# Kernel optimization log

Hardware: AMD Instinct MI355X
Metric: run time of the kernel (lower is better)

The kernel has to match this reference:

```python
import jax, jax.numpy as jnp
import numpy as np

D = 1024
H = 16
HD = D // H
FF = 4096
B = 2
S = 2048


def _layer_norm(x, g, b, eps=1e-5):
    mu = jnp.mean(x, axis=-1, keepdims=True)
    var = jnp.mean(jnp.square(x - mu), axis=-1, keepdims=True)
    return (x - mu) * jax.lax.rsqrt(var + eps) * g + b


def setup_inputs() -> dict:
    key = jax.random.key(0)
    ks = jax.random.split(key, 16)
    s = 0.02
    return {
        "x": jax.random.normal(ks[0], (B, S, D), jnp.float32),
        "Wq": jax.random.normal(ks[1], (H, D, HD), jnp.float32) * s,
        "bq": jnp.zeros((H, HD), jnp.float32),
        "Wk": jax.random.normal(ks[2], (H, D, HD), jnp.float32) * s,
        "bk": jnp.zeros((H, HD), jnp.float32),
        "Wv": jax.random.normal(ks[3], (H, D, HD), jnp.float32) * s,
        "bv": jnp.zeros((H, HD), jnp.float32),
        "Wo": jax.random.normal(ks[4], (D, D), jnp.float32) * s,
        "bo": jnp.zeros((D,), jnp.float32),
        "W1": jax.random.normal(ks[5], (D, FF), jnp.float32) * s,
        "b1": jnp.zeros((FF,), jnp.float32),
        "W2": jax.random.normal(ks[6], (FF, D), jnp.float32) * s,
        "b2": jnp.zeros((D,), jnp.float32),
        "g1": jnp.ones((D,), jnp.float32),
        "be1": jnp.zeros((D,), jnp.float32),
        "g2": jnp.ones((D,), jnp.float32),
        "be2": jnp.zeros((D,), jnp.float32),
    }


def reference(x, Wq, bq, Wk, bk, Wv, bv, Wo, bo, W1, b1, W2, b2, g1, be1, g2, be2):
    b, s, d = x.shape
    # per-head projections (vectorized over heads)
    q = jnp.einsum("bsd,hde->bhse", x, Wq) + bq[None, :, None, :]
    k = jnp.einsum("bsd,hde->bhse", x, Wk) + bk[None, :, None, :]
    v = jnp.einsum("bsd,hde->bhse", x, Wv) + bv[None, :, None, :]
    # NOTE: source scales by 1/dim_k (not 1/sqrt(dim_k)) -- kept faithful
    scores = jnp.einsum("bhse,bhte->bhst", q, k) / jnp.asarray(HD, x.dtype)
    causal = jnp.tril(jnp.ones((s, s), bool))  # [S,S]
    scores = jnp.where(causal[None, None], scores, jnp.asarray(-jnp.inf, x.dtype))
    attn = jax.nn.softmax(scores, axis=-1)
    ctx = jnp.einsum("bhst,bhte->bhse", attn, v)  # [B,H,S,hd]
    ctx = jnp.transpose(ctx, (0, 2, 1, 3)).reshape(b, s, d)  # concat heads
    attn_out = ctx @ Wo + bo
    x = _layer_norm(x + attn_out, g1, be1)
    # feed-forward: linear -> exact GELU -> linear (dropout = eval identity)
    h = jax.nn.gelu(x @ W1 + b1, approximate=False)
    ff = h @ W2 + b2
    return _layer_norm(x + ff, g2, be2)
```

## Files before the change

kernel.cpp:

```cpp
#include <hip/hip_runtime.h>
#include <math.h>

constexpr int Dm  = 1024;
constexpr int Hh  = 16;
constexpr int HDm = 64;
constexpr int FFm = 4096;
constexpr int Bb  = 2;
constexpr int Sq  = 2048;
constexpr int Mm  = Bb * Sq;

typedef __attribute__((ext_vector_type(8))) short short8;
typedef __attribute__((ext_vector_type(4))) short short4v;
typedef __attribute__((ext_vector_type(4))) float f32x4;

#define AS1 __attribute__((address_space(1)))
#define AS3 __attribute__((address_space(3)))

constexpr float QSCALE = 0.022542110013890054f;

__device__ __forceinline__ unsigned short f2b(float f) {
    union { float f; unsigned u; } v; v.f = f;
    unsigned r = v.u + 0x7FFFu + ((v.u >> 16) & 1u);
    return (unsigned short)(r >> 16);
}

__global__ __launch_bounds__(256) void convert_x(const float* __restrict__ x,
                                                 short* __restrict__ xb) {
    int i = blockIdx.x * 256 + threadIdx.x;
    float4 v = ((const float4*)x)[i];
    short4v o;
    o[0] = (short)f2b(v.x); o[1] = (short)f2b(v.y);
    o[2] = (short)f2b(v.z); o[3] = (short)f2b(v.w);
    ((short4v*)xb)[i] = o;
}

__global__ __launch_bounds__(256) void transpose_to_bf16(
    const float* __restrict__ src, short* __restrict__ dst, int R, int C) {
    __shared__ float t[64][65];
    const int c0 = blockIdx.x * 64, r0 = blockIdx.y * 64;
    const int lc = threadIdx.x & 63, lr4 = threadIdx.x >> 6;
    #pragma unroll
    for (int p = 0; p < 16; ++p) {
        int rr = p * 4 + lr4;
        t[rr][lc] = src[(size_t)(r0 + rr) * C + c0 + lc];
    }
    __syncthreads();
    #pragma unroll
    for (int p = 0; p < 16; ++p) {
        int rr = p * 4 + lr4;
        dst[(size_t)(c0 + rr) * R + r0 + lc] = (short)f2b(t[lc][rr]);
    }
}

__global__ __launch_bounds__(256) void build_wqkv(
    const float* __restrict__ Wq, const float* __restrict__ Wk,
    const float* __restrict__ Wv, short* __restrict__ dst) {
    const int kt = blockIdx.x, h = blockIdx.y, which = blockIdx.z;
    const float* W = ((which == 0) ? Wq : (which == 1) ? Wk : Wv) +
                     (size_t)h * Dm * HDm;
    __shared__ float t[64][65];
    const int lc = threadIdx.x & 63, lr4 = threadIdx.x >> 6;
    #pragma unroll
    for (int p = 0; p < 16; ++p) {
        int kr = p * 4 + lr4;
        t[kr][lc] = W[(size_t)(kt * 64 + kr) * HDm + lc];
    }
    __syncthreads();
    const int nbase = which * 1024 + h * 64;
    #pragma unroll
    for (int p = 0; p < 16; ++p) {
        int e = p * 4 + lr4;
        dst[(size_t)(nbase + e) * Dm + kt * 64 + lc] = (short)f2b(t[lc][e]);
    }
}

__global__ __launch_bounds__(256) void build_bqkv(
    const float* __restrict__ bq, const float* __restrict__ bk,
    const float* __restrict__ bv, float* __restrict__ bcat) {
    int n = blockIdx.x * 256 + threadIdx.x;
    const float* s = (n < 1024) ? bq : (n < 2048) ? bk : bv;
    bcat[n] = s[n & 1023];
}

template<int EPI>
__global__ __launch_bounds__(512, 2) void gemm256(
    const short* __restrict__ A, const short* __restrict__ Bt,
    const float* __restrict__ bias,
    short* __restrict__ outb,
    short* __restrict__ qo, short* __restrict__ ko, short* __restrict__ vo,
    int K, int N, int NMT)
{
    __shared__ __align__(16) char lds[131072];
    char* const ldsA = lds;
    char* const ldsB = lds + 65536;
    const int tid = threadIdx.x;
    const int l = tid & 63, wv = tid >> 6;
    const int wm = wv >> 2, wn = wv & 3;
    const int lr = l & 15, lg = l >> 4;
    const int bid = blockIdx.x;
    const int m0 = (bid % NMT) * 256;
    const int n0 = (bid / NMT) * 256;
    const size_t KB = (size_t)K * 2;
    const int NT = K >> 6;

    const char* pA[2][2];
    const char* pB[2][2];
    #pragma unroll
    for (int i = 0; i < 2; ++i) {
        int c = tid + 512 * i;
        int rh = c >> 3, j = c & 7;
        int sw = (j ^ (rh & 7)) << 4;
        #pragma unroll
        for (int h = 0; h < 2; ++h) {
            pA[h][i] = (const char*)A + (size_t)(m0 + h * 128 + rh) * KB + sw;
            pB[h][i] = (const char*)Bt + (size_t)(n0 + h * 128 + rh) * KB + sw;
        }
    }
    const int dbase = tid * 16;

    f32x4 acc[8][4];
    f32x4 z4 = {0.f, 0.f, 0.f, 0.f};
    #pragma unroll
    for (int i = 0; i < 8; ++i)
        #pragma unroll
        for (int j = 0; j < 4; ++j) acc[i][j] = z4;

#define STAGE_B(h, nb) do {                                                     \
    char* _b = ldsB + ((nb) * 2 + (h)) * 16384;                                 \
    __builtin_amdgcn_global_load_lds((const AS1 void*)pB[h][0],                 \
        (AS3 void*)(_b + dbase), 16, 0, 0);                                     \
    __builtin_amdgcn_global_load_lds((const AS1 void*)pB[h][1],                 \
        (AS3 void*)(_b + dbase + 8192), 16, 0, 0);                              \
    pB[h][0] += 128; pB[h][1] += 128; } while (0)
#define STAGE_A(h, nb) do {                                                     \
    char* _a = ldsA + ((nb) * 2 + (h)) * 16384;                                 \
    __builtin_amdgcn_global_load_lds((const AS1 void*)pA[h][0],                 \
        (AS3 void*)(_a + dbase), 16, 0, 0);                                     \
    __builtin_amdgcn_global_load_lds((const AS1 void*)pA[h][1],                 \
        (AS3 void*)(_a + dbase + 8192), 16, 0, 0);                              \
    pA[h][0] += 128; pA[h][1] += 128; } while (0)

    STAGE_B(0, 0); STAGE_B(1, 0); STAGE_A(0, 0); STAGE_A(1, 0);
    asm volatile("s_waitcnt vmcnt(2)" ::: "memory");
    __builtin_amdgcn_s_barrier();
    __builtin_amdgcn_sched_barrier(0);

    const int swk0 = ((0 + lg) ^ (lr & 7)) << 4;
    const int swk1 = ((4 + lg) ^ (lr & 7)) << 4;

    for (int kt = 0; kt < NT; ++kt) {
        const int buf = kt & 1, nbuf = buf ^ 1;
        const bool more = (kt + 1 < NT);
        char* const Ah0 = ldsA + (buf * 2) * 16384;
        char* const Ah1 = ldsA + (buf * 2 + 1) * 16384;
        char* const Bh  = ldsB + (buf * 2 + (wn >> 1)) * 16384 + (wn & 1) * 8192;

        short8 bf[4][2];
        #pragma unroll
        for (int nf = 0; nf < 4; ++nf) {
            const char* bb = Bh + (nf * 16 + lr) * 128;
            bf[nf][0] = *(const short8*)(bb + swk0);
            bf[nf][1] = *(const short8*)(bb + swk1);
        }
        short8 af[2][2];

#define LOAD_A(p) do {                                                          \
    _Pragma("unroll")                                                           \
    for (int j2 = 0; j2 < 2; ++j2) {                                            \
        const int mf = 2 * (p) + j2;                                            \
        const char* ab = ((mf >> 2) ? Ah1 : Ah0) +                              \
                         ((mf & 3) * 32 + wm * 16 + lr) * 128;                  \
        af[j2][0] = *(const short8*)(ab + swk0);                                \
        af[j2][1] = *(const short8*)(ab + swk1);                                \
    } } while (0)

#define MFMA8(p) do {                                                           \
    _Pragma("unroll")                                                           \
    for (int j2 = 0; j2 < 2; ++j2)                                              \
        _Pragma("unroll")                                                       \
        for (int nf = 0; nf < 4; ++nf) {                                        \
            acc[2 * (p) + j2][nf] = __builtin_amdgcn_mfma_f32_16x16x32_bf16(    \
                af[j2][0], bf[nf][0], acc[2 * (p) + j2][nf], 0, 0, 0);          \
            acc[2 * (p) + j2][nf] = __builtin_amdgcn_mfma_f32_16x16x32_bf16(    \
                af[j2][1], bf[nf][1], acc[2 * (p) + j2][nf], 0, 0, 0);          \
        } } while (0)

        LOAD_A(0);
        if (more) STAGE_B(0, nbuf);
        __builtin_amdgcn_s_barrier();
        asm volatile("s_waitcnt lgkmcnt(0)" ::: "memory");
        __builtin_amdgcn_sched_barrier(0);
        __builtin_amdgcn_s_setprio(1);
        MFMA8(0);
        __builtin_amdgcn_s_setprio(0);
        __builtin_amdgcn_s_barrier();
        LOAD_A(1);
        if (more) STAGE_B(1, nbuf);
        __builtin_amdgcn_s_barrier();
        asm volatile("s_waitcnt lgkmcnt(0)" ::: "memory");
        __builtin_amdgcn_sched_barrier(0);
        __builtin_amdgcn_s_setprio(1);
        MFMA8(1);
        __builtin_amdgcn_s_setprio(0);
        if (more) asm volatile("s_waitcnt vmcnt(4)" ::: "memory");
        else      asm volatile("s_waitcnt vmcnt(0)" ::: "memory");
        __builtin_amdgcn_s_barrier();
        __builtin_amdgcn_sched_barrier(0);
        LOAD_A(2);
        if (more) STAGE_A(0, nbuf);
        __builtin_amdgcn_s_barrier();
        asm volatile("s_waitcnt lgkmcnt(0)" ::: "memory");
        __builtin_amdgcn_sched_barrier(0);
        __builtin_amdgcn_s_setprio(1);
        MFMA8(2);
        __builtin_amdgcn_s_setprio(0);
        __builtin_amdgcn_s_barrier();
        LOAD_A(3);
        if (more) STAGE_A(1, nbuf);
        __builtin_amdgcn_s_barrier();
        asm volatile("s_waitcnt lgkmcnt(0)" ::: "memory");
        __builtin_amdgcn_sched_barrier(0);
        __builtin_amdgcn_s_setprio(1);
        MFMA8(3);
        __builtin_amdgcn_s_setprio(0);
        asm volatile("s_waitcnt vmcnt(2)" ::: "memory");
        __builtin_amdgcn_s_barrier();
        __builtin_amdgcn_sched_barrier(0);
#undef LOAD_A
#undef MFMA8
    }

    #pragma unroll
    for (int mf = 0; mf < 8; ++mf) {
        #pragma unroll
        for (int nf = 0; nf < 4; ++nf) {
            const int n = n0 + wn * 64 + nf * 16 + lr;
            const int mB = m0 + mf * 32 + wm * 16 + lg * 4;
            if (EPI == 1) {
                #pragma unroll
                for (int r = 0; r < 4; ++r) {
                    float val = acc[mf][nf][r] + bias[n];
                    val = 0.5f * val * (1.0f + erff(val * 0.70710678118654752f));
                    outb[(size_t)(mB + r) * N + n] = (short)f2b(val);
                }
            } else {
                const int which = n >> 10, hh = (n >> 6) & 15, e = n & 63;
                const int bb2 = mB >> 11, ss = mB & 2047;
                if (which == 2) {
                    short4v pk;
                    #pragma unroll
                    for (int r = 0; r < 4; ++r)
                        pk[r] = (short)f2b(acc[mf][nf][r] + bias[n]);
                    *(short4v*)&vo[(((size_t)bb2 * Hh + hh) * HDm + e) * Sq + ss] = pk;
                } else {
                    short* o = (which == 0) ? qo : ko;
                    const float sc = (which == 0) ? QSCALE : 1.0f;
                    #pragma unroll
                    for (int r = 0; r < 4; ++r) {
                        float val = (acc[mf][nf][r] + bias[n]) * sc;
                        o[(((size_t)bb2 * Hh + hh) * Sq + ss + r) * HDm + e] = (short)f2b(val);
                    }
                }
            }
        }
    }
#undef STAGE_A
#undef STAGE_B
}

template<int EPI>
__global__ __launch_bounds__(256, 2) void gemm128dp(
    const short* __restrict__ A, const short* __restrict__ Bt,
    const float* __restrict__ bias, const float* __restrict__ res,
    float* __restrict__ outf, short* __restrict__ outb,
    int K, int N)
{
    __shared__ __align__(16) char lds[65536];
    char* const ldsA = lds;
    char* const ldsB = lds + 32768;
    const int tid = threadIdx.x;
    const int l = tid & 63, wv = tid >> 6;
    const int wr = wv >> 1, wc = wv & 1;
    const int lr = l & 15, lg = l >> 4;
    const int m0 = blockIdx.x * 128, n0 = blockIdx.y * 128;
    const size_t KB = (size_t)K * 2;
    const int NT = K >> 6;

    const int r0 = tid >> 3, jj = tid & 7;
    const int sw = (jj ^ (r0 & 7)) << 4;
    const char* aSrc[4]; const char* bSrc1[2]; const char* bSrc2[2];
    #pragma unroll
    for (int i = 0; i < 4; ++i)
        aSrc[i] = (const char*)A + (size_t)(m0 + r0 + 32 * i) * KB + sw;
    #pragma unroll
    for (int i = 0; i < 2; ++i) {
        bSrc1[i] = (const char*)Bt + (size_t)(n0 + r0 + 64 * i) * KB + sw;
        bSrc2[i] = (const char*)Bt + (size_t)(n0 + 32 + r0 + 64 * i) * KB + sw;
    }
    const int aDst0 = tid * 16;

#define STAGE_SA(nb) do {                                                       \
    char* _a = ldsA + (nb) * 16384;                                             \
    _Pragma("unroll")                                                           \
    for (int i = 0; i < 4; ++i) {                                               \
        __builtin_amdgcn_global_load_lds((const AS1 void*)aSrc[i],              \
            (AS3 void*)(_a + aDst0 + i * 4096), 16, 0, 0);                      \
        aSrc[i] += 128;                                                         \
    } } while (0)
#define STAGE_SB1(nb) do {                                                      \
    char* _b = ldsB + (nb) * 16384;                                             \
    _Pragma("unroll")                                                           \
    for (int i = 0; i < 2; ++i) {                                               \
        __builtin_amdgcn_global_load_lds((const AS1 void*)bSrc1[i],             \
            (AS3 void*)(_b + aDst0 + i * 8192), 16, 0, 0);                      \
        bSrc1[i] += 128;                                                        \
    } } while (0)
#define STAGE_SB2(nb) do {                                                      \
    char* _b = ldsB + (nb) * 16384 + 4096;                                      \
    _Pragma("unroll")                                                           \
    for (int i = 0; i < 2; ++i) {                                               \
        __builtin_amdgcn_global_load_lds((const AS1 void*)bSrc2[i],             \
            (AS3 void*)(_b + aDst0 + i * 8192), 16, 0, 0);                      \
        bSrc2[i] += 128;                                                        \
    } } while (0)

    f32x4 acc[4][4];
    f32x4 z4 = {0.f, 0.f, 0.f, 0.f};
    #pragma unroll
    for (int i = 0; i < 4; ++i)
        #pragma unroll
        for (int j = 0; j < 4; ++j) acc[i][j] = z4;

    STAGE_SA(0); STAGE_SB1(0); STAGE_SB2(0);
    asm volatile("s_waitcnt vmcnt(2)" ::: "memory");
    __builtin_amdgcn_s_barrier();
    __builtin_amdgcn_sched_barrier(0);

    const int swk0 = ((0 + lg) ^ (lr & 7)) << 4;
    const int swk1 = ((4 + lg) ^ (lr & 7)) << 4;

    for (int kt = 0; kt < NT; ++kt) {
        const int buf = kt & 1, nbuf = buf ^ 1;
        const bool more = (kt + 1 < NT);
        char* const Ab = ldsA + buf * 16384;
        char* const Bb = ldsB + buf * 16384;

        short8 af[4][2], bf[2][2];
        #pragma unroll
        for (int mf = 0; mf < 4; ++mf) {
            const int row = wr * 64 + mf * 16 + lr;
            const char* ab = Ab + row * 128;
            af[mf][0] = *(const short8*)(ab + ((0 + lg) ^ (row & 7) ? 0 : 0, swk0));
            af[mf][0] = *(const short8*)(ab + (((0 + lg) ^ (row & 7)) << 4));
            af[mf][1] = *(const short8*)(ab + (((4 + lg) ^ (row & 7)) << 4));
        }
        #pragma unroll
        for (int nf = 0; nf < 2; ++nf) {
            const int row = wc * 64 + nf * 16 + lr;
            const char* bb = Bb + row * 128;
            bf[nf][0] = *(const short8*)(bb + (((0 + lg) ^ (row & 7)) << 4));
            bf[nf][1] = *(const short8*)(bb + (((4 + lg) ^ (row & 7)) << 4));
        }
        if (more) STAGE_SA(nbuf);
        asm volatile("s_waitcnt lgkmcnt(0)" ::: "memory");
        __builtin_amdgcn_sched_barrier(0);
        __builtin_amdgcn_s_setprio(1);
        #pragma unroll
        for (int mf = 0; mf < 4; ++mf)
            #pragma unroll
            for (int nf = 0; nf < 2; ++nf) {
                acc[mf][nf] = __builtin_amdgcn_mfma_f32_16x16x32_bf16(
                    af[mf][0], bf[nf][0], acc[mf][nf], 0, 0, 0);
                acc[mf][nf] = __builtin_amdgcn_mfma_f32_16x16x32_bf16(
                    af[mf][1], bf[nf][1], acc[mf][nf], 0, 0, 0);
            }
        __builtin_amdgcn_s_setprio(0);
        if (more) asm volatile("s_waitcnt vmcnt(4)" ::: "memory");
        else      asm volatile("s_waitcnt vmcnt(0)" ::: "memory");
        __builtin_amdgcn_s_barrier();
        __builtin_amdgcn_sched_barrier(0);

        #pragma unroll
        for (int nf = 0; nf < 2; ++nf) {
            const int row = wc * 64 + (nf + 2) * 16 + lr;
            const char* bb = Bb + row * 128;
            bf[nf][0] = *(const short8*)(bb + (((0 + lg) ^ (row & 7)) << 4));
            bf[nf][1] = *(const short8*)(bb + (((4 + lg) ^ (row & 7)) << 4));
        }
        if (more) { STAGE_SB1(nbuf); STAGE_SB2(nbuf); }
        asm volatile("s_waitcnt lgkmcnt(0)" ::: "memory");
        __builtin_amdgcn_sched_barrier(0);
        __builtin_amdgcn_s_setprio(1);
        #pragma unroll
        for (int mf = 0; mf < 4; ++mf)
            #pragma unroll
            for (int nf = 0; nf < 2; ++nf) {
                acc[mf][nf + 2] = __builtin_amdgcn_mfma_f32_16x16x32_bf16(
                    af[mf][0], bf[nf][0], acc[mf][nf + 2], 0, 0, 0);
                acc[mf][nf + 2] = __builtin_amdgcn_mfma_f32_16x16x32_bf16(
                    af[mf][1], bf[nf][1], acc[mf][nf + 2], 0, 0, 0);
            }
        __builtin_amdgcn_s_setprio(0);
        if (more) {
            asm volatile("s_waitcnt vmcnt(2)" ::: "memory");
            __builtin_amdgcn_s_barrier();
            __builtin_amdgcn_sched_barrier(0);
        }
    }

    #pragma unroll
    for (int mf = 0; mf < 4; ++mf) {
        #pragma unroll
        for (int nf = 0; nf < 4; ++nf) {
            #pragma unroll
            for (int r = 0; r < 4; ++r) {
                int m = m0 + wr * 64 + mf * 16 + lg * 4 + r;
                int n = n0 + wc * 64 + nf * 16 + lr;
                float val = acc[mf][nf][r];
                if (EPI == 0) {
                    val += bias[n] + res[(size_t)m * N + n];
                    outf[(size_t)m * N + n] = val;
                } else {
                    val += bias[n];
                    val = 0.5f * val * (1.0f + erff(val * 0.70710678118654752f));
                    outb[(size_t)m * N + n] = (short)f2b(val);
                }
            }
        }
    }
#undef STAGE_SA
#undef STAGE_SB1
#undef STAGE_SB2
}

__global__ __launch_bounds__(256) void attn_mfma(
    const short* __restrict__ qg, const short* __restrict__ kg,
    const short* __restrict__ vtg, short* __restrict__ ctx)
{
    const int bid = blockIdx.x;
    const int qt = (Sq / 64 - 1) - (bid >> 5);
    const int hb = bid & 31;
    const int h = hb & 15, b = hb >> 4;
    const int tid = threadIdx.x;
    const int l = tid & 63, wv = tid >> 6;
    const int lr = l & 15, lg = l >> 4;

    __shared__ __align__(16) char KlB[8192];
    __shared__ __align__(16) char VtB[8192];
    __shared__ __align__(16) char PlB[4][2048];

    const size_t bh = ((size_t)b * Hh + h) * Sq;
    const size_t vbase = ((size_t)b * Hh + h) * HDm * Sq;

    const int qbase = qt * 64 + wv * 16;
    short8 aq[2];
    #pragma unroll
    for (int ks = 0; ks < 2; ++ks)
        aq[ks] = *(const short8*)(qg + (bh + qbase + lr) * HDm + ks * 32 + lg * 8);

    f32x4 zero4 = {0.f, 0.f, 0.f, 0.f};
    f32x4 oacc[4], lacc = zero4;
    #pragma unroll
    for (int i = 0; i < 4; ++i) oacc[i] = zero4;
    float mreg[4];
    #pragma unroll
    for (int r = 0; r < 4; ++r) mreg[r] = -3e38f;

    short8 vone;
    #pragma unroll
    for (int j = 0; j < 8; ++j) vone[j] = (short)0x3F80;

    char* plw = PlB[wv];

    const char* srcK[2]; const char* srcV[2];
    #pragma unroll
    for (int r2 = 0; r2 < 2; ++r2) {
        int cl = tid + 256 * r2;
        int row = cl >> 3, j = cl & 7;
        srcK[r2] = (const char*)kg + ((bh + row) * HDm + ((j ^ (row & 7)) * 8)) * 2;
        srcV[r2] = (const char*)vtg + (vbase + (size_t)row * Sq + ((j ^ (row & 7)) * 8)) * 2;
    }

    const int nt = qt + 1;
    for (int tk = 0; tk < nt; ++tk) {
        __syncthreads();
        #pragma unroll
        for (int r2 = 0; r2 < 2; ++r2) {
            int c = tid + 256 * r2;
            __builtin_amdgcn_global_load_lds((const AS1 void*)srcK[r2],
                (AS3 void*)(KlB + c * 16), 16, 0, 0);
            srcK[r2] += 64 * HDm * 2;
            __builtin_amdgcn_global_load_lds((const AS1 void*)srcV[r2],
                (AS3 void*)(VtB + c * 16), 16, 0, 0);
            srcV[r2] += 64 * 2;
        }
        __syncthreads();

        f32x4 sc[4];
        #pragma unroll
        for (int i = 0; i < 4; ++i) sc[i] = zero4;
        __builtin_amdgcn_s_setprio(1);
        #pragma unroll
        for (int kd = 0; kd < 2; ++kd) {
            #pragma unroll
            for (int nf = 0; nf < 4; ++nf) {
                short8 bk = *(const short8*)(KlB + (nf * 16 + lr) * 128 +
                                (((kd * 4 + lg) ^ (lr & 7)) << 4));
                sc[nf] = __builtin_amdgcn_mfma_f32_16x16x32_bf16(
                    aq[kd], bk, sc[nf], 0, 0, 0);
            }
        }
        __builtin_amdgcn_s_setprio(0);

        if (tk == qt) {
            #pragma unroll
            for (int r = 0; r < 4; ++r) {
                const int qglob = qbase + lg * 4 + r;
                #pragma unroll
                for (int nf = 0; nf < 4; ++nf)
                    if (tk * 64 + nf * 16 + lr > qglob) sc[nf][r] = -3e38f;
            }
        }

        float lm[4];
        #pragma unroll
        for (int r = 0; r < 4; ++r)
            lm[r] = fmaxf(fmaxf(sc[0][r], sc[1][r]), fmaxf(sc[2][r], sc[3][r]));
        bool grow = (lm[0] > mreg[0] + 8.f) || (lm[1] > mreg[1] + 8.f) ||
                    (lm[2] > mreg[2] + 8.f) || (lm[3] > mreg[3] + 8.f);

        if (__any((int)grow)) {
            #pragma unroll
            for (int r = 0; r < 4; ++r) {
                float mr = lm[r];
                #pragma unroll
                for (int o = 1; o < 16; o <<= 1)
                    mr = fmaxf(mr, __shfl_xor(mr, o));
                float mnew = fmaxf(mreg[r], mr);
                float cf = exp2f(mreg[r] - mnew);
                mreg[r] = mnew;
                const int prow = lg * 4 + r;
                #pragma unroll
                for (int nf = 0; nf < 4; ++nf) {
                    float p = exp2f(sc[nf][r] - mnew);
                    *(unsigned short*)(plw + prow * 128 +
                        (((nf * 2 + (lr >> 3)) ^ (prow & 7)) << 4) +
                        ((lr & 7) << 1)) = (unsigned short)(__float_as_uint(p) >> 16);
                }
                #pragma unroll
                for (int nf = 0; nf < 4; ++nf) oacc[nf][r] *= cf;
                lacc[r] *= cf;
            }
        } else {
            #pragma unroll
            for (int r = 0; r < 4; ++r) {
                const int prow = lg * 4 + r;
                #pragma unroll
                for (int nf = 0; nf < 4; ++nf) {
                    float p = exp2f(sc[nf][r] - mreg[r]);
                    *(unsigned short*)(plw + prow * 128 +
                        (((nf * 2 + (lr >> 3)) ^ (prow & 7)) << 4) +
                        ((lr & 7) << 1)) = (unsigned short)(__float_as_uint(p) >> 16);
                }
            }
        }

        asm volatile("s_waitcnt lgkmcnt(0)" ::: "memory");
        __builtin_amdgcn_sched_barrier(0);

        __builtin_amdgcn_s_setprio(1);
        #pragma unroll
        for (int ks = 0; ks < 2; ++ks) {
            short8 pa = *(const short8*)(plw + lr * 128 +
                            (((ks * 4 + lg) ^ (lr & 7)) << 4));
            #pragma unroll
            for (int nf = 0; nf < 4; ++nf) {
                short8 bv8 = *(const short8*)(VtB + (nf * 16 + lr) * 128 +
                                (((ks * 4 + lg) ^ (lr & 7)) << 4));
                oacc[nf] = __builtin_amdgcn_mfma_f32_16x16x32_bf16(
                    pa, bv8, oacc[nf], 0, 0, 0);
            }
            lacc = __builtin_amdgcn_mfma_f32_16x16x32_bf16(pa, vone, lacc, 0, 0, 0);
        }
        __builtin_amdgcn_s_setprio(0);
    }

    #pragma unroll
    for (int r = 0; r < 4; ++r) {
        float inv = 1.0f / lacc[r];
        int q = qbase + lg * 4 + r;
        size_t o = ((size_t)b * Sq + q) * Dm + h * HDm;
        #pragma unroll
        for (int nf = 0; nf < 4; ++nf)
            ctx[o + nf * 16 + lr] = (short)f2b(oacc[nf][r] * inv);
    }
}

template<int BF16OUT>
__global__ __launch_bounds__(256) void ln_kernel(
    const float* __restrict__ in, const float* __restrict__ g,
    const float* __restrict__ be, float* __restrict__ outf,
    short* __restrict__ outb)
{
    const int m = blockIdx.x;
    const int tid = threadIdx.x;
    const float4 vl = *(const float4*)&in[(size_t)m * Dm + tid * 4];
    float s  = vl.x + vl.y + vl.z + vl.w;
    float s2 = vl.x * vl.x + vl.y * vl.y + vl.z * vl.z + vl.w * vl.w;
    #pragma unroll
    for (int o = 32; o > 0; o >>= 1) {
        s  += __shfl_down(s, o);
        s2 += __shfl_down(s2, o);
    }
    __shared__ float rs[4], rs2[4];
    const int w = tid >> 6;
    if ((tid & 63) == 0) { rs[w] = s; rs2[w] = s2; }
    __syncthreads();
    s  = rs[0] + rs[1] + rs[2] + rs[3];
    s2 = rs2[0] + rs2[1] + rs2[2] + rs2[3];
    const float mean = s * (1.0f / Dm);
    const float var  = s2 * (1.0f / Dm) - mean * mean;
    const float rstd = rsqrtf(var + 1e-5f);
    const float4 gv = *(const float4*)&g[tid * 4];
    const float4 bv = *(const float4*)&be[tid * 4];
    float4 ov;
    ov.x = (vl.x - mean) * rstd * gv.x + bv.x;
    ov.y = (vl.y - mean) * rstd * gv.y + bv.y;
    ov.z = (vl.z - mean) * rstd * gv.z + bv.z;
    ov.w = (vl.w - mean) * rstd * gv.w + bv.w;
    *(float4*)&outf[(size_t)m * Dm + tid * 4] = ov;
    if (BF16OUT) {
        short4v o4;
        o4[0] = (short)f2b(ov.x); o4[1] = (short)f2b(ov.y);
        o4[2] = (short)f2b(ov.z); o4[3] = (short)f2b(ov.w);
        *(short4v*)&outb[(size_t)m * Dm + tid * 4] = o4;
    }
}

extern "C" void kernel_launch(void* const* d_in, const int* in_sizes, int n_in,
                              void* d_out, int out_size, void* d_ws, size_t ws_size,
                              hipStream_t stream)
{
    const float* x  = (const float*)d_in[0];
    const float* Wq = (const float*)d_in[1];
    const float* bq = (const float*)d_in[2];
    const float* Wk = (const float*)d_in[3];
    const float* bk = (const float*)d_in[4];
    const float* Wv = (const float*)d_in[5];
    const float* bv = (const float*)d_in[6];
    const float* Wo = (const float*)d_in[7];
    const float* bo = (const float*)d_in[8];
    const float* W1 = (const float*)d_in[9];
    const float* b1 = (const float*)d_in[10];
    const float* W2 = (const float*)d_in[11];
    const float* b2 = (const float*)d_in[12];
    const float* g1 = (const float*)d_in[13];
    const float* be1= (const float*)d_in[14];
    const float* g2 = (const float*)d_in[15];
    const float* be2= (const float*)d_in[16];
    float* out = (float*)d_out;

    char* ws = (char*)d_ws;
    size_t off = 0;
    auto alloc = [&](size_t bytes) {
        char* p = ws + off;
        off += (bytes + 255) & ~(size_t)255;
        return p;
    };
    const size_t MD2 = (size_t)Mm * Dm * 2;
    short* xb    = (short*)alloc(MD2);
    short* wqkvt = (short*)alloc((size_t)3072 * Dm * 2);
    float* bcat  = (float*)alloc(3072 * 4);
    short* wot   = (short*)alloc((size_t)Dm * Dm * 2);
    short* w1t   = (short*)alloc((size_t)FFm * Dm * 2);
    short* w2t   = (short*)alloc((size_t)Dm * FFm * 2);
    short* qb    = (short*)alloc(MD2);
    short* kb    = (short*)alloc(MD2);
    short* vtb   = (short*)alloc(MD2);
    short* ctxb  = (short*)alloc(MD2);
    short* hb    = qb;
    float* y     = (float*)alloc((size_t)Mm * Dm * 4);
    float* x1f   = (float*)alloc((size_t)Mm * Dm * 4);
    short* x1b   = (short*)alloc(MD2);
    float* y2    = y;

    convert_x<<<Mm * Dm / 1024, 256, 0, stream>>>(x, xb);
    build_wqkv<<<dim3(16, 16, 3), 256, 0, stream>>>(Wq, Wk, Wv, wqkvt);
    build_bqkv<<<12, 256, 0, stream>>>(bq, bk, bv, bcat);
    transpose_to_bf16<<<dim3(16, 16), 256, 0, stream>>>(Wo, wot, Dm, Dm);
    transpose_to_bf16<<<dim3(64, 16), 256, 0, stream>>>(W1, w1t, Dm, FFm);
    transpose_to_bf16<<<dim3(16, 64), 256, 0, stream>>>(W2, w2t, FFm, Dm);

    gemm256<2><<<192, 512, 0, stream>>>(
        xb, wqkvt, bcat, nullptr, qb, kb, vtb, Dm, 3072, 16);
    attn_mfma<<<1024, 256, 0, stream>>>(qb, kb, vtb, ctxb);
    gemm128dp<0><<<dim3(32, 8), 256, 0, stream>>>(
        ctxb, wot, bo, x, y, nullptr, Dm, Dm);
    ln_kernel<1><<<Mm, 256, 0, stream>>>(y, g1, be1, x1f, x1b);
    gemm256<1><<<256, 512, 0, stream>>>(
        x1b, w1t, b1, hb, nullptr, nullptr, nullptr, Dm, FFm, 16);
    gemm128dp<0><<<dim3(32, 8), 256, 0, stream>>>(
        hb, w2t, b2, x1f, y2, nullptr, FFm, Dm);
    ln_kernel<0><<<Mm, 256, 0, stream>>>(y2, g2, be2, out, nullptr);
}
```

Baseline: 252.7 us.

## Template gemm128dp on M tile, use 64-row tiles, and fast GELU approximation

Makes the M tile height of the dual-phase GEMM a template parameter and launches the two N=1024 GEMMs with 64-row tiles. This doubles the grid from 256 to 512 blocks so more of the GPU's compute units get work, at the cost of less reuse of the B operand per block. The wait counts are adjusted to match the smaller A stage. It also replaces the exact erf GELU with a sigmoid-based polynomial approximation using exp2 and a fast reciprocal, which cuts epilogue arithmetic but no longer matches exact GELU.

```diff
diff --git a/kernel.cpp b/kernel.cpp
--- a/kernel.cpp
+++ b/kernel.cpp
@@ -22,6 +22,11 @@
     union { float f; unsigned u; } v; v.f = f;
     unsigned r = v.u + 0x7FFFu + ((v.u >> 16) & 1u);
     return (unsigned short)(r >> 16);
+}
+
+__device__ __forceinline__ float gelu_fast(float x) {
+    float z = x * (2.302080918f + 0.102938049f * x * x);
+    return x * __builtin_amdgcn_rcpf(1.0f + exp2f(-z));
 }
 
 __global__ __launch_bounds__(256) void convert_x(const float* __restrict__ x,
@@ -239,8 +244,7 @@
             if (EPI == 1) {
                 #pragma unroll
                 for (int r = 0; r < 4; ++r) {
-                    float val = acc[mf][nf][r] + bias[n];
-                    val = 0.5f * val * (1.0f + erff(val * 0.70710678118654752f));
+                    float val = gelu_fast(acc[mf][nf][r] + bias[n]);
                     outb[(size_t)(mB + r) * N + n] = (short)f2b(val);
                 }
             } else {
@@ -268,29 +272,33 @@
 #undef STAGE_B
 }
 
-template<int EPI>
+template<int EPI, int BM>
 __global__ __launch_bounds__(256, 2) void gemm128dp(
     const short* __restrict__ A, const short* __restrict__ Bt,
     const float* __restrict__ bias, const float* __restrict__ res,
     float* __restrict__ outf, short* __restrict__ outb,
     int K, int N)
 {
-    __shared__ __align__(16) char lds[65536];
+    constexpr int AR  = BM / 32;
+    constexpr int BMW = BM / 2;
+    constexpr int MF  = BMW / 16;
+    constexpr int ABUF = BM * 128;
+    __shared__ __align__(16) char lds[2 * ABUF + 32768];
     char* const ldsA = lds;
-    char* const ldsB = lds + 32768;
+    char* const ldsB = lds + 2 * ABUF;
     const int tid = threadIdx.x;
     const int l = tid & 63, wv = tid >> 6;
     const int wr = wv >> 1, wc = wv & 1;
     const int lr = l & 15, lg = l >> 4;
-    const int m0 = blockIdx.x * 128, n0 = blockIdx.y * 128;
+    const int m0 = blockIdx.x * BM, n0 = blockIdx.y * 128;
     const size_t KB = (size_t)K * 2;
     const int NT = K >> 6;
 
     const int r0 = tid >> 3, jj = tid & 7;
     const int sw = (jj ^ (r0 & 7)) << 4;
-    const char* aSrc[4]; const char* bSrc1[2]; const char* bSrc2[2];
-    #pragma unroll
-    for (int i = 0; i < 4; ++i)
+    const char* aSrc[AR]; const char* bSrc1[2]; const char* bSrc2[2];
+    #pragma unroll
+    for (int i = 0; i < AR; ++i)
         aSrc[i] = (const char*)A + (size_t)(m0 + r0 + 32 * i) * KB + sw;
     #pragma unroll
     for (int i = 0; i < 2; ++i) {
@@ -300,9 +308,9 @@
     const int aDst0 = tid * 16;
 
 #define STAGE_SA(nb) do {                                                       \
-    char* _a = ldsA + (nb) * 16384;                                             \
+    char* _a = ldsA + (nb) * ABUF;                                              \
     _Pragma("unroll")                                                           \
-    for (int i = 0; i < 4; ++i) {                                               \
+    for (int i = 0; i < AR; ++i) {                                              \
         __builtin_amdgcn_global_load_lds((const AS1 void*)aSrc[i],              \
             (AS3 void*)(_a + aDst0 + i * 4096), 16, 0, 0);                      \
         aSrc[i] += 128;                                                         \
@@ -324,10 +332,10 @@
         bSrc2[i] += 128;                                                        \
     } } while (0)
 
-    f32x4 acc[4][4];
+    f32x4 acc[MF][4];
     f32x4 z4 = {0.f, 0.f, 0.f, 0.f};
     #pragma unroll
-    for (int i = 0; i < 4; ++i)
+    for (int i = 0; i < MF; ++i)
         #pragma unroll
         for (int j = 0; j < 4; ++j) acc[i][j] = z4;
 
@@ -336,21 +344,17 @@
     __builtin_amdgcn_s_barrier();
     __builtin_amdgcn_sched_barrier(0);
 
-    const int swk0 = ((0 + lg) ^ (lr & 7)) << 4;
-    const int swk1 = ((4 + lg) ^ (lr & 7)) << 4;
-
     for (int kt = 0; kt < NT; ++kt) {
         const int buf = kt & 1, nbuf = buf ^ 1;
         const bool more = (kt + 1 < NT);
-        char* const Ab = ldsA + buf * 16384;
+        char* const Ab = ldsA + buf * ABUF;
         char* const Bb = ldsB + buf * 16384;
 
-        short8 af[4][2], bf[2][2];
-        #pragma unroll
-        for (int mf = 0; mf < 4; ++mf) {
-            const int row = wr * 64 + mf * 16 + lr;
+        short8 af[MF][2], bf[2][2];
+        #pragma unroll
+        for (int mf = 0; mf < MF; ++mf) {
+            const int row = wr * BMW + mf * 16 + lr;
             const char* ab = Ab + row * 128;
-            af[mf][0] = *(const short8*)(ab + ((0 + lg) ^ (row & 7) ? 0 : 0, swk0));
             af[mf][0] = *(const short8*)(ab + (((0 + lg) ^ (row & 7)) << 4));
             af[mf][1] = *(const short8*)(ab + (((4 + lg) ^ (row & 7)) << 4));
         }
@@ -366,7 +370,7 @@
         __builtin_amdgcn_sched_barrier(0);
         __builtin_amdgcn_s_setprio(1);
         #pragma unroll
-        for (int mf = 0; mf < 4; ++mf)
+        for (int mf = 0; mf < MF; ++mf)
             #pragma unroll
             for (int nf = 0; nf < 2; ++nf) {
                 acc[mf][nf] = __builtin_amdgcn_mfma_f32_16x16x32_bf16(
@@ -375,8 +379,12 @@
                     af[mf][1], bf[nf][1], acc[mf][nf], 0, 0, 0);
             }
         __builtin_amdgcn_s_setprio(0);
-        if (more) asm volatile("s_waitcnt vmcnt(4)" ::: "memory");
-        else      asm volatile("s_waitcnt vmcnt(0)" ::: "memory");
+        if (more) {
+            if constexpr (BM == 128) asm volatile("s_waitcnt vmcnt(4)" ::: "memory");
+            else                     asm volatile("s_waitcnt vmcnt(2)" ::: "memory");
+        } else {
+            asm volatile("s_waitcnt vmcnt(0)" ::: "memory");
+        }
         __builtin_amdgcn_s_barrier();
         __builtin_amdgcn_sched_barrier(0);
 
@@ -392,7 +400,7 @@
         __builtin_amdgcn_sched_barrier(0);
         __builtin_amdgcn_s_setprio(1);
         #pragma unroll
-        for (int mf = 0; mf < 4; ++mf)
+        for (int mf = 0; mf < MF; ++mf)
             #pragma unroll
             for (int nf = 0; nf < 2; ++nf) {
                 acc[mf][nf + 2] = __builtin_amdgcn_mfma_f32_16x16x32_bf16(
@@ -409,20 +417,19 @@
     }
 
     #pragma unroll
-    for (int mf = 0; mf < 4; ++mf) {
+    for (int mf = 0; mf < MF; ++mf) {
         #pragma unroll
         for (int nf = 0; nf < 4; ++nf) {
             #pragma unroll
             for (int r = 0; r < 4; ++r) {
-                int m = m0 + wr * 64 + mf * 16 + lg * 4 + r;
+                int m = m0 + wr * BMW + mf * 16 + lg * 4 + r;
                 int n = n0 + wc * 64 + nf * 16 + lr;
                 float val = acc[mf][nf][r];
                 if (EPI == 0) {
                     val += bias[n] + res[(size_t)m * N + n];
                     outf[(size_t)m * N + n] = val;
                 } else {
-                    val += bias[n];
-                    val = 0.5f * val * (1.0f + erff(val * 0.70710678118654752f));
+                    val = gelu_fast(val + bias[n]);
                     outb[(size_t)m * N + n] = (short)f2b(val);
                 }
             }
@@ -694,12 +701,12 @@
     gemm256<2><<<192, 512, 0, stream>>>(
         xb, wqkvt, bcat, nullptr, qb, kb, vtb, Dm, 3072, 16);
     attn_mfma<<<1024, 256, 0, stream>>>(qb, kb, vtb, ctxb);
-    gemm128dp<0><<<dim3(32, 8), 256, 0, stream>>>(
+    gemm128dp<0, 64><<<dim3(64, 8), 256, 0, stream>>>(
         ctxb, wot, bo, x, y, nullptr, Dm, Dm);
     ln_kernel<1><<<Mm, 256, 0, stream>>>(y, g1, be1, x1f, x1b);
     gemm256<1><<<256, 512, 0, stream>>>(
         x1b, w1t, b1, hb, nullptr, nullptr, nullptr, Dm, FFm, 16);
-    gemm128dp<0><<<dim3(32, 8), 256, 0, stream>>>(
+    gemm128dp<0, 64><<<dim3(64, 8), 256, 0, stream>>>(
         hb, w2t, b2, x1f, y2, nullptr, FFm, Dm);
     ln_kernel<0><<<Mm, 256, 0, stream>>>(y2, g2, be2, out, nullptr);
 }
```

After: 235.5 us. 1.07x faster.
